# Kernel optimization log

Hardware: AMD Instinct MI355X
Metric: run time of the kernel (lower is better)

Reference implementation:

```python
import jax, jax.numpy as jnp
import numpy as np

# ---- config (matches init_kwargs) ----
M, N, D = 8, 512, 243            # meshes, neurons per mesh, input dim
E_RATIO = 0.8
NE = int(N * E_RATIO)            # 409 excitatory
NI = N - NE                      # 103 inhibitory
TICKS = 16
BATCH = 512
BITS = 4
WSCALE = 8.0
VTH, VRESET = 1.0, 0.0
TAU_E, TAU_I, DT = 2.0, 1.5, 1.0
BETA = 10.0                      # fast-sigmoid surrogate slope
INPUT_SCALE = 1.0


def fake_quant(w):
    """Quantization-aware fake quant with straight-through estimator."""
    step = WSCALE / (2 ** (BITS - 1))          # 1.0 for 4-bit, scale 8
    q = jnp.clip(jnp.round(w / step), -(2 ** (BITS - 1)), 2 ** (BITS - 1) - 1) * step
    return w + jax.lax.stop_gradient(q - w)


@jax.custom_vjp
def spike(u):
    return (u >= 0.0).astype(u.dtype)

def _spike_fwd(u):
    return spike(u), u

def _spike_bwd(u, g):
    # fast-sigmoid surrogate gradient
    return (g * BETA / (1.0 + BETA * jnp.abs(u)) ** 2,)

spike.defvjp(_spike_fwd, _spike_bwd)


def setup_inputs() -> dict:
    key = jax.random.key(0)
    ks = jax.random.split(key, 8)

    def sparse_w(k, shape, density, std, zero_diag=False):
        km, kw = jax.random.split(k)
        mask = (jax.random.uniform(km, shape) < density).astype(jnp.float32)
        if zero_diag:
            mask = mask * (1.0 - jnp.eye(shape[-1], dtype=jnp.float32))
        return jax.random.normal(kw, shape) * std * mask

    x = jax.random.normal(ks[0], (BATCH, D), dtype=jnp.float32)
    W_in = jax.random.normal(ks[1], (M, N, D)) * 0.8      # per-mesh input projection [out,in]
    b_in = jax.random.normal(ks[2], (M, N)) * 0.05
    W_inter = sparse_w(ks[3], (M, N, NE), 0.3, 0.8)        # inter-mesh: E of mesh m -> mesh m+1
    W_EE = sparse_w(ks[4], (M, NE, NE), 0.5, 0.8, True)
    W_EI = sparse_w(ks[5], (M, NI, NE), 0.6, 0.8)
    W_IE = sparse_w(ks[6], (M, NE, NI), 0.8, 0.8)
    W_II = sparse_w(ks[7], (M, NI, NI), 0.7, 0.8, True)
    return dict(x=x, W_in=W_in, b_in=b_in, W_inter=W_inter,
                W_EE=W_EE, W_EI=W_EI, W_IE=W_IE, W_II=W_II)


def reference(x, W_in, b_in, W_inter, W_EE, W_EI, W_IE, W_II):
    B = x.shape[0]
    decay_E = 1.0 - DT / TAU_E
    decay_I = 1.0 - DT / TAU_I

    # quantize weights once (constant across ticks)
    qW_in, qW_inter = fake_quant(W_in), fake_quant(W_inter)
    qW_EE, qW_EI = fake_quant(W_EE), fake_quant(W_EI)
    qW_IE, qW_II = fake_quant(W_IE), fake_quant(W_II)

    # external input projection, same every tick: [M, B, N]
    ext_proj = jnp.einsum('bd,mnd->mbn', x * INPUT_SCALE, qW_in) + b_in[:, None, :]

    def tick(carry, _):
        e, i, vE, vI, acc = carry          # e:[M,B,NE] i:[M,B,NI]
        # inter-mesh: mesh m receives inter_connections[m-1](e_prev[m-1])
        inter = jnp.einsum('mbe,mne->mbn', e, qW_inter)
        ext = ext_proj + jnp.roll(inter, 1, axis=0)
        cE = ext[:, :, :NE] \
            + jnp.einsum('mbe,mfe->mbf', e, qW_EE) \
            + jnp.einsum('mbi,mfi->mbf', i, qW_IE)
        cI = ext[:, :, NE:] \
            + jnp.einsum('mbe,mfe->mbf', e, qW_EI) \
            + jnp.einsum('mbi,mfi->mbf', i, qW_II)
        # LIF: leaky decay + input, threshold, hard reset
        vE = vE * decay_E + cE * DT
        vI = vI * decay_I + cI * DT
        sE = spike(vE - VTH)
        sI = spike(vI - VTH)
        vE = sE * VRESET + (1.0 - sE) * vE
        vI = sI * VRESET + (1.0 - sI) * vI
        acc = acc + jnp.concatenate([sE, sI], axis=-1)
        return (sE, sI, vE, vI, acc), None

    z = jnp.zeros
    carry0 = (z((M, B, NE)), z((M, B, NI)), z((M, B, NE)), z((M, B, NI)), z((M, B, N)))
    (eF, iF, vEF, vIF, acc), _ = jax.lax.scan(tick, carry0, None, length=TICKS)
    # accumulator laid out mesh-major: [B, M*N]
    return jnp.transpose(acc, (1, 0, 2)).reshape(B, M * N)
```

## Files before the change

### kernel.cpp

```cpp
#include <hip/hip_runtime.h>
#include <hip/hip_bf16.h>

#define Mm 8
#define Nn 512
#define NEe 409
#define NIi 103
#define Bb 512
#define Dd 243
#define Tt 16
#define SPROW 640
#define WCROW 1152
#define DEC_I 0.33333334f
#define NBLK 256
#define FLAGSTRIDE 16
#define FLAGINTS 8192
#define SPINMAX 1000000L

typedef int v4i __attribute__((ext_vector_type(4)));
union LV { long l[2]; v4i v; };

__device__ __forceinline__ float quantf(float w) {
    float q = rintf(w);
    return fminf(fmaxf(q, -8.0f), 7.0f);
}

__global__ void k_pack(const float* __restrict__ Wint, const float* __restrict__ WEE,
                       const float* __restrict__ WEI, const float* __restrict__ WIE,
                       const float* __restrict__ WII, signed char* __restrict__ Wc,
                       int* __restrict__ flags) {
    if (blockIdx.x == 0) {
        for (int i = threadIdx.x; i < FLAGINTS; i += 256) flags[i] = 0;
    }
    int q = blockIdx.x * 256 + threadIdx.x;
    if (q >= (Mm * Nn * WCROW) / 4) return;
    int k0 = (q * 4) % WCROW;
    int n  = ((q * 4) / WCROW) & (Nn - 1);
    int m  = (q * 4) / (WCROW * Nn);
    char out4[4];
#pragma unroll
    for (int j = 0; j < 4; ++j) {
        int k = k0 + j;
        float w = 0.0f;
        if (k < 512) {
            if (k < NEe) w = Wint[((((m + 7) & 7) * Nn) + n) * NEe + k];
        } else if (k < 1024) {
            int jj = k - 512;
            if (jj < NEe) w = (n < NEe) ? WEE[((m * NEe) + n) * NEe + jj]
                                        : WEI[((m * NIi) + (n - NEe)) * NEe + jj];
        } else {
            int jj = k - 1024;
            if (jj < NIi) w = (n < NEe) ? WIE[((m * NEe) + n) * NIi + jj]
                                        : WII[((m * NIi) + (n - NEe)) * NIi + jj];
        }
        out4[j] = (signed char)(int)quantf(w);
    }
    *(int*)&Wc[q * 4] = *(int*)out4;
}

__global__ void k_ext(const float* __restrict__ x, const float* __restrict__ Win,
                      const float* __restrict__ bin, float* __restrict__ ext) {
    __shared__ float xs[64][68];
    __shared__ float wsm[64][68];
    const int bid = blockIdx.x;
    const int m  = bid >> 6;
    const int bt = (bid >> 3) & 7;
    const int nt = bid & 7;
    const int b0 = bt * 64, n0 = nt * 64;
    const int t = threadIdx.x;
    const int tb4 = (t & 15) * 4;
    const int tn4 = (t >> 4) * 4;
    const int sr = t >> 2;
    const int sc = (t & 3) * 16;
    float c[4][4];
#pragma unroll
    for (int i = 0; i < 4; ++i)
#pragma unroll
        for (int j = 0; j < 4; ++j) c[i][j] = 0.0f;

    for (int d0 = 0; d0 < Dd; d0 += 64) {
#pragma unroll
        for (int j = 0; j < 16; ++j) {
            int d = d0 + sc + j;
            float xv = 0.0f, wv = 0.0f;
            if (d < Dd) {
                xv = x[(b0 + sr) * Dd + d];
                wv = quantf(Win[((m * Nn) + n0 + sr) * Dd + d]);
            }
            xs[sc + j][sr] = xv;
            wsm[sc + j][sr] = wv;
        }
        __syncthreads();
        const int dmax = min(64, Dd - d0);
        for (int d = 0; d < dmax; ++d) {
            float4 av = *(const float4*)&xs[d][tb4];
            float4 wv = *(const float4*)&wsm[d][tn4];
            float a[4] = {av.x, av.y, av.z, av.w};
            float wq[4] = {wv.x, wv.y, wv.z, wv.w};
#pragma unroll
            for (int i = 0; i < 4; ++i)
#pragma unroll
                for (int j = 0; j < 4; ++j)
                    c[i][j] = fmaf(a[i], wq[j], c[i][j]);
        }
        __syncthreads();
    }
#pragma unroll
    for (int i = 0; i < 4; ++i)
#pragma unroll
        for (int j = 0; j < 4; ++j) {
            float val = __fadd_rn(c[i][j], bin[m * Nn + n0 + tn4 + j]);
            ext[(size_t)(m * Bb + b0 + tb4 + i) * Nn + n0 + tn4 + j] = val;
        }
}

__global__ void __launch_bounds__(512, 2)
k_ticks(const signed char* __restrict__ Wc,
        signed char* __restrict__ Sp0,
        signed char* __restrict__ Sp1,
        const float* __restrict__ ext,
        float* __restrict__ out,
        int* __restrict__ flags) {
    __shared__ __align__(16) signed char sA[2][64][256];
    __shared__ __align__(16) signed char sB[2][128][256];

    const int wg = blockIdx.x;
    const int m  = wg & 7;
    const int bt = (wg >> 3) & 7;
    const int nt = wg >> 6;
    const int b0 = bt * 64;
    const int n0 = nt * 128;
    const int pm = (m + 7) & 7;
    const int nm = (m + 1) & 7;

    const int tid  = threadIdx.x;
    const int w    = tid >> 6;
    const int lane = tid & 63;
    const int bh   = w & 1;
    const int nh   = w >> 1;
    const int quad = lane >> 4;
    const int li   = lane & 15;

    int waitIdx = 0;
    if (tid < 12) {
        int g  = tid >> 2;
        int mm = (g == 0) ? pm : ((g == 1) ? m : nm);
        waitIdx = (((tid & 3) << 6) | (bt << 3) | mm) * FLAGSTRIDE;
    }

    int rowA[2], cnkA[2], gcolA[2], scolA[2];
#pragma unroll
    for (int j = 0; j < 2; ++j) {
        int ch = tid + j * 512;
        rowA[j]  = ch >> 4;
        cnkA[j]  = ch & 15;
        gcolA[j] = cnkA[j] * 16;
        scolA[j] = (cnkA[j] ^ (rowA[j] & 15)) * 16;
    }
    int rowB[4], cnkB[4], gcolB[4], scolB[4];
#pragma unroll
    for (int j = 0; j < 4; ++j) {
        int ch = tid + j * 512;
        rowB[j]  = ch >> 4;
        cnkB[j]  = ch & 15;
        gcolB[j] = cnkB[j] * 16;
        scolB[j] = (cnkB[j] ^ (rowB[j] & 15)) * 16;
    }

    float decs[2]; int offs[2]; int nels[2];
#pragma unroll
    for (int tn = 0; tn < 2; ++tn) {
        int n = n0 + nh * 32 + tn * 16 + li;
        nels[tn] = n;
        decs[tn] = (n < NEe) ? 0.5f : DEC_I;
        offs[tn] = (n < NEe) ? n : (n + 103);
    }
    const int bbase = b0 + bh * 32;

    const signed char* WcBase = Wc + (size_t)(m * Nn + n0) * WCROW;

    float extr[2][2][4];
#pragma unroll
    for (int tb = 0; tb < 2; ++tb)
#pragma unroll
        for (int tn = 0; tn < 2; ++tn)
#pragma unroll
            for (int r = 0; r < 4; ++r) {
                int b = bbase + tb * 16 + quad * 4 + r;
                extr[tb][tn][r] = ext[(size_t)(m * Bb + b) * Nn + nels[tn]];
            }
    float vmem[2][2][4];
    int cnt[2][2];
#pragma unroll
    for (int tb = 0; tb < 2; ++tb)
#pragma unroll
        for (int tn = 0; tn < 2; ++tn) {
            cnt[tb][tn] = 0;
#pragma unroll
            for (int r = 0; r < 4; ++r) vmem[tb][tn][r] = 0.0f;
        }

    if (nt == 0) {
        for (int idx = tid; idx < 64 * 128 * 2; idx += 512) {
            int bufsel = idx >> 13;
            int rr = (idx >> 7) & 63;
            int p  = idx & 127;
            int off = (p < 103) ? (409 + p) : (615 + (p - 103));
            signed char* base = (bufsel ? Sp1 : Sp0) + (size_t)(m * Bb + b0 + rr) * SPROW + off;
            __hip_atomic_store(base, (signed char)0, __ATOMIC_RELAXED, __HIP_MEMORY_SCOPE_AGENT);
        }
    }

    for (int t = 0; t < Tt; ++t) {
        signed char* SR = (t & 1) ? Sp1 : Sp0;
        signed char* SW = (t & 1) ? Sp0 : Sp1;
        signed char* AbasePrev = SR + (size_t)(pm * Bb + b0) * SPROW;
        signed char* AbaseOwn  = SR + (size_t)(m  * Bb + b0) * SPROW;

        if (t > 0) {
            if (tid < 12) {
                long spin = 0;
                while (__hip_atomic_load(&flags[waitIdx],
                                         __ATOMIC_RELAXED, __HIP_MEMORY_SCOPE_AGENT) < t) {
                    __builtin_amdgcn_s_sleep(2);
                    if (++spin > SPINMAX) break;
                }
            }
            __syncthreads();
        }

        float c[2][2][4];

        if (t == 0) {
#pragma unroll
            for (int tb = 0; tb < 2; ++tb)
#pragma unroll
                for (int tn = 0; tn < 2; ++tn)
#pragma unroll
                    for (int r = 0; r < 4; ++r)
                        c[tb][tn][r] = __fadd_rn(__fadd_rn(__fadd_rn(extr[tb][tn][r], 0.0f), 0.0f), 0.0f);
        } else {
            v4i acc[2][2];
#pragma unroll
            for (int tb = 0; tb < 2; ++tb)
#pragma unroll
                for (int tn = 0; tn < 2; ++tn) acc[tb][tn] = (v4i){0, 0, 0, 0};

#pragma unroll
            for (int j = 0; j < 2; ++j) {
                long* ap = (long*)(AbasePrev + (size_t)rowA[j] * SPROW + gcolA[j]);
                LV tmp;
                tmp.l[0] = __hip_atomic_load(ap,     __ATOMIC_RELAXED, __HIP_MEMORY_SCOPE_AGENT);
                tmp.l[1] = __hip_atomic_load(ap + 1, __ATOMIC_RELAXED, __HIP_MEMORY_SCOPE_AGENT);
                *(v4i*)&sA[0][rowA[j]][scolA[j]] = tmp.v;
            }
#pragma unroll
            for (int j = 0; j < 4; ++j)
                *(v4i*)&sB[0][rowB[j]][scolB[j]] =
                    *(const v4i*)(WcBase + (size_t)rowB[j] * WCROW + gcolB[j]);
            __syncthreads();

            for (int it = 0; it < 4; ++it) {
                const int buf = it & 1;
                const int k0 = (it + 1) * 256;
                signed char* ab; int ko;
                if (k0 < 512) { ab = AbasePrev; ko = k0; }
                else          { ab = AbaseOwn;  ko = k0 - 512; }
                const int kw = (it == 3) ? 128 : 256;
                v4i nA[2], nB[4];
                bool ldA[2], ldB[4];
#pragma unroll
                for (int j = 0; j < 2; ++j) {
                    ldA[j] = (gcolA[j] < kw);
                    if (ldA[j]) {
                        long* ap = (long*)(ab + (size_t)rowA[j] * SPROW + ko + gcolA[j]);
                        LV tmp;
                        tmp.l[0] = __hip_atomic_load(ap,     __ATOMIC_RELAXED, __HIP_MEMORY_SCOPE_AGENT);
                        tmp.l[1] = __hip_atomic_load(ap + 1, __ATOMIC_RELAXED, __HIP_MEMORY_SCOPE_AGENT);
                        nA[j] = tmp.v;
                    }
                }
#pragma unroll
                for (int j = 0; j < 4; ++j) {
                    ldB[j] = (gcolB[j] < kw);
                    if (ldB[j])
                        nB[j] = *(const v4i*)(WcBase + (size_t)rowB[j] * WCROW + k0 + gcolB[j]);
                }
#pragma unroll
                for (int ks = 0; ks < 256; ks += 64) {
                    const int c0 = (((ks >> 4) + quad) ^ li) * 16;
                    v4i af0 = *(const v4i*)&sA[buf][bh * 32 + li][c0];
                    v4i af1 = *(const v4i*)&sA[buf][bh * 32 + 16 + li][c0];
#pragma unroll
                    for (int tn = 0; tn < 2; ++tn) {
                        v4i bfr = *(const v4i*)&sB[buf][nh * 32 + tn * 16 + li][c0];
                        acc[0][tn] = __builtin_amdgcn_mfma_i32_16x16x64_i8(af0, bfr, acc[0][tn], 0, 0, 0);
                        acc[1][tn] = __builtin_amdgcn_mfma_i32_16x16x64_i8(af1, bfr, acc[1][tn], 0, 0, 0);
                    }
                }
                const int nb = buf ^ 1;
#pragma unroll
                for (int j = 0; j < 2; ++j)
                    if (ldA[j]) *(v4i*)&sA[nb][rowA[j]][scolA[j]] = nA[j];
#pragma unroll
                for (int j = 0; j < 4; ++j)
                    if (ldB[j]) *(v4i*)&sB[nb][rowB[j]][scolB[j]] = nB[j];
                __syncthreads();
                if (it == 1) {
#pragma unroll
                    for (int tb = 0; tb < 2; ++tb)
#pragma unroll
                        for (int tn = 0; tn < 2; ++tn) {
#pragma unroll
                            for (int r = 0; r < 4; ++r)
                                c[tb][tn][r] = __fadd_rn(extr[tb][tn][r], (float)acc[tb][tn][r]);
                            acc[tb][tn] = (v4i){0, 0, 0, 0};
                        }
                } else if (it == 3) {
#pragma unroll
                    for (int tb = 0; tb < 2; ++tb)
#pragma unroll
                        for (int tn = 0; tn < 2; ++tn) {
#pragma unroll
                            for (int r = 0; r < 4; ++r)
                                c[tb][tn][r] = __fadd_rn(c[tb][tn][r], (float)acc[tb][tn][r]);
                            acc[tb][tn] = (v4i){0, 0, 0, 0};
                        }
                }
            }
#pragma unroll
            for (int ks = 0; ks < 128; ks += 64) {
                const int c0 = (((ks >> 4) + quad) ^ li) * 16;
                v4i af0 = *(const v4i*)&sA[0][bh * 32 + li][c0];
                v4i af1 = *(const v4i*)&sA[0][bh * 32 + 16 + li][c0];
#pragma unroll
                for (int tn = 0; tn < 2; ++tn) {
                    v4i bfr = *(const v4i*)&sB[0][nh * 32 + tn * 16 + li][c0];
                    acc[0][tn] = __builtin_amdgcn_mfma_i32_16x16x64_i8(af0, bfr, acc[0][tn], 0, 0, 0);
                    acc[1][tn] = __builtin_amdgcn_mfma_i32_16x16x64_i8(af1, bfr, acc[1][tn], 0, 0, 0);
                }
            }
#pragma unroll
            for (int tb = 0; tb < 2; ++tb)
#pragma unroll
                for (int tn = 0; tn < 2; ++tn)
#pragma unroll
                    for (int r = 0; r < 4; ++r)
                        c[tb][tn][r] = __fadd_rn(c[tb][tn][r], (float)acc[tb][tn][r]);
        }

#pragma unroll
        for (int tb = 0; tb < 2; ++tb)
#pragma unroll
            for (int tn = 0; tn < 2; ++tn)
#pragma unroll
                for (int r = 0; r < 4; ++r) {
                    float vn = __fadd_rn(__fmul_rn(vmem[tb][tn][r], decs[tn]), c[tb][tn][r]);
                    int s = (vn >= 1.0f) ? 1 : 0;
                    vmem[tb][tn][r] = s ? 0.0f : vn;
                    cnt[tb][tn] += s << (r * 8);
                    if (t < Tt - 1) {
                        int b = bbase + tb * 16 + quad * 4 + r;
                        signed char* sp = SW + (size_t)(m * Bb + b) * SPROW + offs[tn];
                        __hip_atomic_store(sp, (signed char)s,
                                           __ATOMIC_RELAXED, __HIP_MEMORY_SCOPE_AGENT);
                    }
                }
        if (t < Tt - 1) {
            __syncthreads();
            if (tid == 0)
                __hip_atomic_store(&flags[wg * FLAGSTRIDE], t + 1,
                                   __ATOMIC_RELAXED, __HIP_MEMORY_SCOPE_AGENT);
        }
    }

#pragma unroll
    for (int tb = 0; tb < 2; ++tb)
#pragma unroll
        for (int tn = 0; tn < 2; ++tn)
#pragma unroll
            for (int r = 0; r < 4; ++r) {
                int b = bbase + tb * 16 + quad * 4 + r;
                out[(size_t)b * (Mm * Nn) + m * Nn + nels[tn]] =
                    (float)((cnt[tb][tn] >> (r * 8)) & 0xff);
            }
}

extern "C" void kernel_launch(void* const* d_in, const int* in_sizes, int n_in,
                              void* d_out, int out_size, void* d_ws, size_t ws_size,
                              hipStream_t stream) {
    const float* x    = (const float*)d_in[0];
    const float* Win  = (const float*)d_in[1];
    const float* bin  = (const float*)d_in[2];
    const float* Wint = (const float*)d_in[3];
    const float* WEE  = (const float*)d_in[4];
    const float* WEI  = (const float*)d_in[5];
    const float* WIE  = (const float*)d_in[6];
    const float* WII  = (const float*)d_in[7];
    float* out = (float*)d_out;

    char* ws = (char*)d_ws;
    signed char* Wc  = (signed char*)ws;
    signed char* Sp0 = (signed char*)(ws + 4718592);
    signed char* Sp1 = Sp0 + 2621440;
    int* flags = (int*)(ws + 4718592 + 2 * 2621440);
    float* extw = (float*)(ws + 4718592 + 2 * 2621440 + 32768);

    k_pack<<<(Mm * Nn * WCROW / 4 + 255) / 256, 256, 0, stream>>>(Wint, WEE, WEI, WIE, WII, Wc, flags);
    k_ext<<<512, 256, 0, stream>>>(x, Win, bin, extw);
    k_ticks<<<NBLK, 512, 0, stream>>>(Wc, Sp0, Sp1, (const float*)extw, out, flags);
}
```

Measured before the change: 224.9 us.

## Bit-pack spike exchange and keep weight tile resident in LDS across ticks

Spikes are now exchanged between workgroups as packed bits (96 bytes per row) written with wave ballots, and unpacked into int8 MFMA operands in registers. Before, each tick wrote and read one byte per neuron. The block's 128x1152 int8 weight slice is loaded into shared memory once before the tick loop instead of being streamed from global memory every tick. This drops the double-buffered k-loop and most per-tick barriers. In exchange it adds ALU work for unpacking, needs a large LDS allocation (about 158KB) that may cut occupancy against launch_bounds(512,2), and adds special handling for the E/I boundary word.

```diff
diff --git a/kernel.cpp b/kernel.cpp
--- a/kernel.cpp
+++ b/kernel.cpp
@@ -8,20 +8,30 @@
 #define Bb 512
 #define Dd 243
 #define Tt 16
-#define SPROW 640
+#define SPB 96
 #define WCROW 1152
 #define DEC_I 0.33333334f
 #define NBLK 256
 #define FLAGSTRIDE 16
 #define FLAGINTS 8192
 #define SPINMAX 1000000L
+#define ABROW 176
 
 typedef int v4i __attribute__((ext_vector_type(4)));
-union LV { long l[2]; v4i v; };
 
 __device__ __forceinline__ float quantf(float w) {
     float q = rintf(w);
     return fminf(fmaxf(q, -8.0f), 7.0f);
+}
+
+__device__ __forceinline__ v4i unpack16(unsigned int dl, unsigned int dh, bool qhi, int qsh) {
+    unsigned int d = qhi ? dh : dl;
+    v4i r;
+    r[0] = (int)((((d >> qsh) & 0xFu) * 0x00204081u) & 0x01010101u);
+    r[1] = (int)((((d >> (qsh + 4)) & 0xFu) * 0x00204081u) & 0x01010101u);
+    r[2] = (int)((((d >> (qsh + 8)) & 0xFu) * 0x00204081u) & 0x01010101u);
+    r[3] = (int)((((d >> (qsh + 12)) & 0xFu) * 0x00204081u) & 0x01010101u);
+    return r;
 }
 
 __global__ void k_pack(const float* __restrict__ Wint, const float* __restrict__ WEE,
@@ -48,8 +58,8 @@
             if (jj < NEe) w = (n < NEe) ? WEE[((m * NEe) + n) * NEe + jj]
                                         : WEI[((m * NIi) + (n - NEe)) * NEe + jj];
         } else {
-            int jj = k - 1024;
-            if (jj < NIi) w = (n < NEe) ? WIE[((m * NEe) + n) * NIi + jj]
+            int jj = k - 1049;
+            if (jj >= 0 && jj < NIi) w = (n < NEe) ? WIE[((m * NEe) + n) * NIi + jj]
                                         : WII[((m * NIi) + (n - NEe)) * NIi + jj];
         }
         out4[j] = (signed char)(int)quantf(w);
@@ -115,13 +125,13 @@
 
 __global__ void __launch_bounds__(512, 2)
 k_ticks(const signed char* __restrict__ Wc,
-        signed char* __restrict__ Sp0,
-        signed char* __restrict__ Sp1,
+        unsigned char* __restrict__ Sp0,
+        unsigned char* __restrict__ Sp1,
         const float* __restrict__ ext,
         float* __restrict__ out,
         int* __restrict__ flags) {
-    __shared__ __align__(16) signed char sA[2][64][256];
-    __shared__ __align__(16) signed char sB[2][128][256];
+    __shared__ __align__(16) signed char sB[128 * WCROW];
+    __shared__ __align__(16) unsigned char sAb[64 * ABROW];
 
     const int wg = blockIdx.x;
     const int m  = wg & 7;
@@ -147,36 +157,30 @@
         waitIdx = (((tid & 3) << 6) | (bt << 3) | mm) * FLAGSTRIDE;
     }
 
-    int rowA[2], cnkA[2], gcolA[2], scolA[2];
-#pragma unroll
-    for (int j = 0; j < 2; ++j) {
-        int ch = tid + j * 512;
-        rowA[j]  = ch >> 4;
-        cnkA[j]  = ch & 15;
-        gcolA[j] = cnkA[j] * 16;
-        scolA[j] = (cnkA[j] ^ (rowA[j] & 15)) * 16;
-    }
-    int rowB[4], cnkB[4], gcolB[4], scolB[4];
-#pragma unroll
-    for (int j = 0; j < 4; ++j) {
-        int ch = tid + j * 512;
-        rowB[j]  = ch >> 4;
-        cnkB[j]  = ch & 15;
-        gcolB[j] = cnkB[j] * 16;
-        scolB[j] = (cnkB[j] ^ (rowB[j] & 15)) * 16;
-    }
-
-    float decs[2]; int offs[2]; int nels[2];
+    const signed char* WcBase = Wc + (size_t)(m * Nn + n0) * WCROW;
+#pragma unroll
+    for (int j = 0; j < 18; ++j) {
+        int task = tid + j * 512;
+        int row = task / 72, gg = task % 72;
+        v4i v = *(const v4i*)(WcBase + (size_t)row * WCROW + gg * 16);
+        int gs = (gg < 64) ? ((gg & 48) | ((gg ^ row) & 15))
+                           : (64 + ((gg ^ row) & 7));
+        *(v4i*)&sB[row * WCROW + gs * 16] = v;
+    }
+
+    float decs[2]; int nels[2];
+    int styp[2], soff[2];
 #pragma unroll
     for (int tn = 0; tn < 2; ++tn) {
         int n = n0 + nh * 32 + tn * 16 + li;
         nels[tn] = n;
         decs[tn] = (n < NEe) ? 0.5f : DEC_I;
-        offs[tn] = (n < NEe) ? n : (n + 103);
+        int nb = n0 + nh * 32 + tn * 16;
+        if (nb < 400)      { styp[tn] = 0; soff[tn] = nb >> 3; }
+        else if (nb == 400){ styp[tn] = 2; soff[tn] = 50; }
+        else               { styp[tn] = 1; soff[tn] = 64 + ((nb - 384) >> 3); }
     }
     const int bbase = b0 + bh * 32;
-
-    const signed char* WcBase = Wc + (size_t)(m * Nn + n0) * WCROW;
 
     float extr[2][2][4];
 #pragma unroll
@@ -199,22 +203,23 @@
             for (int r = 0; r < 4; ++r) vmem[tb][tn][r] = 0.0f;
         }
 
-    if (nt == 0) {
-        for (int idx = tid; idx < 64 * 128 * 2; idx += 512) {
-            int bufsel = idx >> 13;
-            int rr = (idx >> 7) & 63;
-            int p  = idx & 127;
-            int off = (p < 103) ? (409 + p) : (615 + (p - 103));
-            signed char* base = (bufsel ? Sp1 : Sp0) + (size_t)(m * Bb + b0 + rr) * SPROW + off;
-            __hip_atomic_store(base, (signed char)0, __ATOMIC_RELAXED, __HIP_MEMORY_SCOPE_AGENT);
-        }
-    }
+    if (nt == 0 && tid < 128) {
+        int buf = tid >> 6, rr = tid & 63;
+        unsigned char* base = (buf ? Sp1 : Sp0) + (size_t)(m * Bb + b0 + rr) * SPB;
+        __hip_atomic_store((unsigned int*)(base + 52), 0u, __ATOMIC_RELAXED, __HIP_MEMORY_SCOPE_AGENT);
+        __hip_atomic_store((unsigned int*)(base + 56), 0u, __ATOMIC_RELAXED, __HIP_MEMORY_SCOPE_AGENT);
+        __hip_atomic_store((unsigned int*)(base + 60), 0u, __ATOMIC_RELAXED, __HIP_MEMORY_SCOPE_AGENT);
+        __hip_atomic_store((unsigned short*)(base + 64), (unsigned short)0, __ATOMIC_RELAXED, __HIP_MEMORY_SCOPE_AGENT);
+    }
+
+    const bool qhi = (quad >= 2);
+    const int qsh = (quad & 1) << 4;
+    const int r0base = (bh * 32 + li) * ABROW;
+    const int r1base = (bh * 32 + 16 + li) * ABROW;
 
     for (int t = 0; t < Tt; ++t) {
-        signed char* SR = (t & 1) ? Sp1 : Sp0;
-        signed char* SW = (t & 1) ? Sp0 : Sp1;
-        signed char* AbasePrev = SR + (size_t)(pm * Bb + b0) * SPROW;
-        signed char* AbaseOwn  = SR + (size_t)(m  * Bb + b0) * SPROW;
+        unsigned char* SR = (t & 1) ? Sp1 : Sp0;
+        unsigned char* SW = (t & 1) ? Sp0 : Sp1;
 
         if (t > 0) {
             if (tid < 12) {
@@ -239,6 +244,25 @@
                     for (int r = 0; r < 4; ++r)
                         c[tb][tn][r] = __fadd_rn(__fadd_rn(__fadd_rn(extr[tb][tn][r], 0.0f), 0.0f), 0.0f);
         } else {
+            const unsigned char* PrevRow = SR + (size_t)(pm * Bb + b0) * SPB;
+            const unsigned char* OwnRow  = SR + (size_t)(m  * Bb + b0) * SPB;
+#pragma unroll
+            for (int j = 0; j < 3; ++j) {
+                int task = tid + j * 512;
+                if (task < 1152) {
+                    int row = task / 18, s = task % 18;
+                    const unsigned char* src;
+                    int dstoff;
+                    if (s < 8)       { src = PrevRow + (size_t)row * SPB + s * 8;            dstoff = s * 8; }
+                    else if (s < 16) { src = OwnRow  + (size_t)row * SPB + (s - 8) * 8;      dstoff = s * 8; }
+                    else             { src = OwnRow  + (size_t)row * SPB + 64 + (s - 16) * 8; dstoff = 128 + (s - 16) * 8; }
+                    unsigned long long vb = __hip_atomic_load((const unsigned long long*)src,
+                                               __ATOMIC_RELAXED, __HIP_MEMORY_SCOPE_AGENT);
+                    *(unsigned long long*)&sAb[row * ABROW + dstoff] = vb;
+                }
+            }
+            __syncthreads();
+
             v4i acc[2][2];
 #pragma unroll
             for (int tb = 0; tb < 2; ++tb)
@@ -246,66 +270,28 @@
                 for (int tn = 0; tn < 2; ++tn) acc[tb][tn] = (v4i){0, 0, 0, 0};
 
 #pragma unroll
-            for (int j = 0; j < 2; ++j) {
-                long* ap = (long*)(AbasePrev + (size_t)rowA[j] * SPROW + gcolA[j]);
-                LV tmp;
-                tmp.l[0] = __hip_atomic_load(ap,     __ATOMIC_RELAXED, __HIP_MEMORY_SCOPE_AGENT);
-                tmp.l[1] = __hip_atomic_load(ap + 1, __ATOMIC_RELAXED, __HIP_MEMORY_SCOPE_AGENT);
-                *(v4i*)&sA[0][rowA[j]][scolA[j]] = tmp.v;
-            }
-#pragma unroll
-            for (int j = 0; j < 4; ++j)
-                *(v4i*)&sB[0][rowB[j]][scolB[j]] =
-                    *(const v4i*)(WcBase + (size_t)rowB[j] * WCROW + gcolB[j]);
-            __syncthreads();
-
-            for (int it = 0; it < 4; ++it) {
-                const int buf = it & 1;
-                const int k0 = (it + 1) * 256;
-                signed char* ab; int ko;
-                if (k0 < 512) { ab = AbasePrev; ko = k0; }
-                else          { ab = AbaseOwn;  ko = k0 - 512; }
-                const int kw = (it == 3) ? 128 : 256;
-                v4i nA[2], nB[4];
-                bool ldA[2], ldB[4];
-#pragma unroll
-                for (int j = 0; j < 2; ++j) {
-                    ldA[j] = (gcolA[j] < kw);
-                    if (ldA[j]) {
-                        long* ap = (long*)(ab + (size_t)rowA[j] * SPROW + ko + gcolA[j]);
-                        LV tmp;
-                        tmp.l[0] = __hip_atomic_load(ap,     __ATOMIC_RELAXED, __HIP_MEMORY_SCOPE_AGENT);
-                        tmp.l[1] = __hip_atomic_load(ap + 1, __ATOMIC_RELAXED, __HIP_MEMORY_SCOPE_AGENT);
-                        nA[j] = tmp.v;
-                    }
-                }
-#pragma unroll
-                for (int j = 0; j < 4; ++j) {
-                    ldB[j] = (gcolB[j] < kw);
-                    if (ldB[j])
-                        nB[j] = *(const v4i*)(WcBase + (size_t)rowB[j] * WCROW + k0 + gcolB[j]);
-                }
+            for (int ch = 0; ch < 4; ++ch) {
+                const int cb = ch << 8;
+                v4i a0lo = *(const v4i*)&sAb[r0base + (cb >> 3)];
+                v4i a0hi = *(const v4i*)&sAb[r0base + (cb >> 3) + 16];
+                v4i a1lo = *(const v4i*)&sAb[r1base + (cb >> 3)];
+                v4i a1hi = *(const v4i*)&sAb[r1base + (cb >> 3) + 16];
 #pragma unroll
                 for (int ks = 0; ks < 256; ks += 64) {
-                    const int c0 = (((ks >> 4) + quad) ^ li) * 16;
-                    v4i af0 = *(const v4i*)&sA[buf][bh * 32 + li][c0];
-                    v4i af1 = *(const v4i*)&sA[buf][bh * 32 + 16 + li][c0];
+                    v4i s0 = (ks < 128) ? a0lo : a0hi;
+                    v4i s1 = (ks < 128) ? a1lo : a1hi;
+                    const int D0 = ((ks >> 6) & 1) ? 2 : 0;
+                    v4i af0 = unpack16((unsigned int)s0[D0], (unsigned int)s0[D0 + 1], qhi, qsh);
+                    v4i af1 = unpack16((unsigned int)s1[D0], (unsigned int)s1[D0 + 1], qhi, qsh);
+                    const int gs = (cb >> 4) + ((((ks >> 4) + quad) ^ li) & 15);
 #pragma unroll
                     for (int tn = 0; tn < 2; ++tn) {
-                        v4i bfr = *(const v4i*)&sB[buf][nh * 32 + tn * 16 + li][c0];
+                        const v4i bfr = *(const v4i*)&sB[(nh * 32 + tn * 16 + li) * WCROW + gs * 16];
                         acc[0][tn] = __builtin_amdgcn_mfma_i32_16x16x64_i8(af0, bfr, acc[0][tn], 0, 0, 0);
                         acc[1][tn] = __builtin_amdgcn_mfma_i32_16x16x64_i8(af1, bfr, acc[1][tn], 0, 0, 0);
                     }
                 }
-                const int nb = buf ^ 1;
-#pragma unroll
-                for (int j = 0; j < 2; ++j)
-                    if (ldA[j]) *(v4i*)&sA[nb][rowA[j]][scolA[j]] = nA[j];
-#pragma unroll
-                for (int j = 0; j < 4; ++j)
-                    if (ldB[j]) *(v4i*)&sB[nb][rowB[j]][scolB[j]] = nB[j];
-                __syncthreads();
-                if (it == 1) {
+                if (ch == 1) {
 #pragma unroll
                     for (int tb = 0; tb < 2; ++tb)
 #pragma unroll
@@ -315,7 +301,7 @@
                                 c[tb][tn][r] = __fadd_rn(extr[tb][tn][r], (float)acc[tb][tn][r]);
                             acc[tb][tn] = (v4i){0, 0, 0, 0};
                         }
-                } else if (it == 3) {
+                } else if (ch == 3) {
 #pragma unroll
                     for (int tb = 0; tb < 2; ++tb)
 #pragma unroll
@@ -327,16 +313,21 @@
                         }
                 }
             }
-#pragma unroll
-            for (int ks = 0; ks < 128; ks += 64) {
-                const int c0 = (((ks >> 4) + quad) ^ li) * 16;
-                v4i af0 = *(const v4i*)&sA[0][bh * 32 + li][c0];
-                v4i af1 = *(const v4i*)&sA[0][bh * 32 + 16 + li][c0];
-#pragma unroll
-                for (int tn = 0; tn < 2; ++tn) {
-                    v4i bfr = *(const v4i*)&sB[0][nh * 32 + tn * 16 + li][c0];
-                    acc[0][tn] = __builtin_amdgcn_mfma_i32_16x16x64_i8(af0, bfr, acc[0][tn], 0, 0, 0);
-                    acc[1][tn] = __builtin_amdgcn_mfma_i32_16x16x64_i8(af1, bfr, acc[1][tn], 0, 0, 0);
+            {
+                v4i e0 = *(const v4i*)&sAb[r0base + 128];
+                v4i e1 = *(const v4i*)&sAb[r1base + 128];
+#pragma unroll
+                for (int ks = 0; ks < 128; ks += 64) {
+                    const int D0 = (ks >> 6) ? 2 : 0;
+                    v4i af0 = unpack16((unsigned int)e0[D0], (unsigned int)e0[D0 + 1], qhi, qsh);
+                    v4i af1 = unpack16((unsigned int)e1[D0], (unsigned int)e1[D0 + 1], qhi, qsh);
+                    const int gs = 64 + ((((ks >> 4) + quad) ^ li) & 7);
+#pragma unroll
+                    for (int tn = 0; tn < 2; ++tn) {
+                        const v4i bfr = *(const v4i*)&sB[(nh * 32 + tn * 16 + li) * WCROW + gs * 16];
+                        acc[0][tn] = __builtin_amdgcn_mfma_i32_16x16x64_i8(af0, bfr, acc[0][tn], 0, 0, 0);
+                        acc[1][tn] = __builtin_amdgcn_mfma_i32_16x16x64_i8(af1, bfr, acc[1][tn], 0, 0, 0);
+                    }
                 }
             }
 #pragma unroll
@@ -348,6 +339,7 @@
                         c[tb][tn][r] = __fadd_rn(c[tb][tn][r], (float)acc[tb][tn][r]);
         }
 
+        int snow[2][2] = {{0, 0}, {0, 0}};
 #pragma unroll
         for (int tb = 0; tb < 2; ++tb)
 #pragma unroll
@@ -358,13 +350,36 @@
                     int s = (vn >= 1.0f) ? 1 : 0;
                     vmem[tb][tn][r] = s ? 0.0f : vn;
                     cnt[tb][tn] += s << (r * 8);
-                    if (t < Tt - 1) {
-                        int b = bbase + tb * 16 + quad * 4 + r;
-                        signed char* sp = SW + (size_t)(m * Bb + b) * SPROW + offs[tn];
-                        __hip_atomic_store(sp, (signed char)s,
-                                           __ATOMIC_RELAXED, __HIP_MEMORY_SCOPE_AGENT);
+                    snow[tb][tn] |= s << r;
+                }
+
+        if (t < Tt - 1) {
+#pragma unroll
+            for (int tb = 0; tb < 2; ++tb)
+#pragma unroll
+                for (int tn = 0; tn < 2; ++tn)
+#pragma unroll
+                    for (int r = 0; r < 4; ++r) {
+                        unsigned long long mk = __ballot((snow[tb][tn] >> r) & 1);
+                        if (li == 0) {
+                            unsigned short v = (unsigned short)(mk >> (unsigned)(quad << 4));
+                            int row = bbase + tb * 16 + quad * 4 + r;
+                            unsigned char* rb = SW + (size_t)(m * Bb + row) * SPB;
+                            if (styp[tn] != 2) {
+                                __hip_atomic_store((unsigned short*)(rb + soff[tn]), v,
+                                                   __ATOMIC_RELAXED, __HIP_MEMORY_SCOPE_AGENT);
+                            } else {
+                                __hip_atomic_store((unsigned short*)(rb + 50),
+                                                   (unsigned short)(v & 0x01FF),
+                                                   __ATOMIC_RELAXED, __HIP_MEMORY_SCOPE_AGENT);
+                                __hip_atomic_store((unsigned short*)(rb + 66),
+                                                   (unsigned short)(v & 0xFE00),
+                                                   __ATOMIC_RELAXED, __HIP_MEMORY_SCOPE_AGENT);
+                            }
+                        }
                     }
-                }
+        }
+
         if (t < Tt - 1) {
             __syncthreads();
             if (tid == 0)
@@ -399,9 +414,9 @@
     float* out = (float*)d_out;
 
     char* ws = (char*)d_ws;
-    signed char* Wc  = (signed char*)ws;
-    signed char* Sp0 = (signed char*)(ws + 4718592);
-    signed char* Sp1 = Sp0 + 2621440;
+    signed char* Wc    = (signed char*)ws;
+    unsigned char* Sp0 = (unsigned char*)(ws + 4718592);
+    unsigned char* Sp1 = Sp0 + 2621440;
     int* flags = (int*)(ws + 4718592 + 2 * 2621440);
     float* extw = (float*)(ws + 4718592 + 2 * 2621440 + 32768);
 
```

New measurement: 203.4 us. 9.5% less time.
